# Kernel tuning notes

Measured on AMD Instinct MI355X. Metric: run time of the kernel, lower is better.

## Reference

```python
import jax, jax.numpy as jnp
import numpy as np
from jax import lax

L, B, N_IN, N_OUT, K = 1024, 16, 1024, 512, 5


def setup_inputs() -> dict:
    key = jax.random.key(0)
    k0, k1, k2, k3, k4 = jax.random.split(key, 5)
    val_range = (6.0 / (N_IN + N_OUT)) ** 0.5
    x = jax.random.normal(k0, (L, B, N_IN), dtype=jnp.float32)
    weight = jax.random.uniform(k1, (N_IN, N_OUT * K), dtype=jnp.float32,
                                minval=-val_range, maxval=val_range)
    bias = jax.random.normal(k2, (N_OUT * K,), dtype=jnp.float32) * 0.1
    bias_eps = jax.random.normal(k3, (N_OUT,), dtype=jnp.float32) * 0.1
    bias_final = jax.random.normal(k4, (N_OUT * 2,), dtype=jnp.float32) * 0.1
    return {"x": x, "weight": weight, "bias": bias,
            "bias_eps": bias_eps, "bias_final": bias_final}


def reference(x, weight, bias, bias_eps, bias_final):
    # x: [L, B, n_in]; unidirectional (bidir=1), real semiring, output gate, tanh
    length, batch, n_in = x.shape
    n_out = N_OUT
    u_ = (x.reshape(-1, n_in) @ weight).reshape(length, batch, n_out, K)
    b = bias.reshape(K, n_out)  # [5, n_out]: in1, in2, f1, f2, out
    forget_bias1, forget_bias2, output_bias = b[2], b[3], b[4]
    output = jax.nn.sigmoid(u_[..., 4] + output_bias)      # [L, B, n_out]
    forget1 = jax.nn.sigmoid(u_[..., 2] + forget_bias1)
    forget2 = jax.nn.sigmoid(u_[..., 3] + forget_bias2)
    u1, u2 = u_[..., 0], u_[..., 1]
    eps = jax.nn.sigmoid(bias_eps)                          # [n_out]

    def step(carry, inp):
        c1_prev, c2_prev = carry
        f1t, f2t, u1t, u2t = inp
        c1_t = c1_prev * f1t + u1t
        c2_t = c2_prev * f2t + (eps + c1_prev) * u2t
        return (c1_t, c2_t), (c1_t, c2_t)

    init = (jnp.zeros((batch, n_out), x.dtype), jnp.zeros((batch, n_out), x.dtype))
    (c1_final, c2_final), (c1s, c2s) = lax.scan(step, init, (forget1, forget2, u1, u2))

    rho = jax.nn.sigmoid(bias_final.reshape(n_out, 2)) * 2.0
    cs = c1s * rho[:, 0] + c2s * rho[:, 1]
    gcs = jnp.tanh(output * cs)                             # [L, B, n_out]
    return gcs, c1_final, c2_final
```

## Files before the change

kernel.cpp:

```cpp
#include <hip/hip_runtime.h>
#include <cstdint>

#define LSEQ 1024
#define BATCH 16
#define NIN 1024
#define NOUT 512
#define KGATE 5
#define NCOL (NOUT * KGATE)
#define MTOT (LSEQ * BATCH)
#define CHAINS (BATCH * NOUT)
#define OUT_GCS (LSEQ * BATCH * NOUT)
#define SEG 32
#define SLEN 32
#define PLANE ((size_t)MTOT * NOUT)
#define SMP ((size_t)SEG * CHAINS)

typedef _Float16 f16x8 __attribute__((ext_vector_type(8)));
typedef float f32x4 __attribute__((ext_vector_type(4)));

__device__ __forceinline__ void async16(const void* g, void* l) {
    __builtin_amdgcn_global_load_lds(
        (const __attribute__((address_space(1))) void*)(uintptr_t)g,
        (__attribute__((address_space(3))) void*)(uintptr_t)l,
        16, 0, 0);
}

__device__ __forceinline__ float fsigmoid(float x) {
    return 1.0f / (1.0f + __expf(-x));
}

__global__ void convert_x_k(const float* __restrict__ x, _Float16* __restrict__ xb, int n8) {
    int i = blockIdx.x * blockDim.x + threadIdx.x;
    if (i < n8) {
        float4 a = ((const float4*)x)[2 * i];
        float4 b = ((const float4*)x)[2 * i + 1];
        f16x8 h;
        h[0] = (_Float16)a.x; h[1] = (_Float16)a.y; h[2] = (_Float16)a.z; h[3] = (_Float16)a.w;
        h[4] = (_Float16)b.x; h[5] = (_Float16)b.y; h[6] = (_Float16)b.z; h[7] = (_Float16)b.w;
        ((f16x8*)xb)[i] = h;
    }
}

__global__ __launch_bounds__(256) void transpose_w_k(const float* __restrict__ w, _Float16* __restrict__ wT) {
    __shared__ float lds[32][33];
    int t = threadIdx.x;
    int col = t & 31;
    int rowg = t >> 5;
    int n0 = blockIdx.x * 32;
    int k0 = blockIdx.y * 32;
#pragma unroll
    for (int i = 0; i < 4; i++) {
        int r = rowg + i * 8;
        lds[r][col] = w[(size_t)(k0 + r) * NCOL + n0 + col];
    }
    __syncthreads();
#pragma unroll
    for (int i = 0; i < 4; i++) {
        int r = rowg + i * 8;
        int c = n0 + r;
        int row = (c % 5) * NOUT + (c / 5);
        wT[(size_t)row * NIN + k0 + col] = (_Float16)lds[col][r];
    }
}

__global__ __launch_bounds__(256, 2) void gemm_gates_k(const _Float16* __restrict__ A,
                                                       const _Float16* __restrict__ BT,
                                                       const float* __restrict__ bias,
                                                       _Float16* __restrict__ planes) {
    __shared__ _Float16 Al[256 * 64];
    __shared__ _Float16 Bl[128 * 64];
    int t = threadIdx.x;
    int w = t >> 6, lane = t & 63;
    int m0 = blockIdx.x * 256, n0 = blockIdx.y * 128;

    f32x4 acc[8][4] = {};

    const int q = lane >> 4, r16 = lane & 15;
    const int wm = (w >> 1) * 128, wn = (w & 1) * 64;

    for (int kk = 0; kk < NIN; kk += 64) {
#pragma unroll
        for (int cc = 0; cc < 8; cc++) {
            int c = t + cc * 256;
            int r = c >> 3, sg = c & 7;
            async16(A + (size_t)(m0 + r) * NIN + kk + sg * 8, (char*)Al + c * 16);
        }
#pragma unroll
        for (int cc = 0; cc < 4; cc++) {
            int c = t + cc * 256;
            int r = c >> 3, sg = c & 7;
            async16(BT + (size_t)(n0 + r) * NIN + kk + sg * 8, (char*)Bl + c * 16);
        }
        __syncthreads();

#pragma unroll
        for (int h = 0; h < 2; h++) {
            f16x8 af[8], bf[4];
#pragma unroll
            for (int i = 0; i < 8; i++)
                af[i] = *(const f16x8*)(Al + (wm + i * 16 + r16) * 64 + h * 32 + q * 8);
#pragma unroll
            for (int j = 0; j < 4; j++)
                bf[j] = *(const f16x8*)(Bl + (wn + j * 16 + r16) * 64 + h * 32 + q * 8);
#pragma unroll
            for (int i = 0; i < 8; i++)
#pragma unroll
                for (int j = 0; j < 4; j++)
                    acc[i][j] = __builtin_amdgcn_mfma_f32_16x16x32_f16(af[i], bf[j], acc[i][j], 0, 0, 0);
        }
        __syncthreads();
    }

    int g = n0 >> 9;
    int nb = n0 & (NOUT - 1);
    _Float16* plane = planes + (size_t)g * PLANE;
#pragma unroll
    for (int j = 0; j < 4; j++) {
        int coln = nb + wn + j * 16 + r16;
        float bv = bias[n0 + wn + j * 16 + r16];
#pragma unroll
        for (int i = 0; i < 8; i++) {
#pragma unroll
            for (int reg = 0; reg < 4; reg++) {
                int m = m0 + wm + i * 16 + q * 4 + reg;
                float v = acc[i][j][reg];
                if (g >= 2) v = fsigmoid(v + bv);
                plane[(size_t)m * NOUT + coln] = (_Float16)v;
            }
        }
    }
}

__global__ __launch_bounds__(256) void compose_k(const _Float16* __restrict__ planes,
                                                 const float* __restrict__ beps,
                                                 float* __restrict__ SM) {
    int u = blockIdx.x * 256 + threadIdx.x;
    int t = u & (CHAINS - 1);
    int s = u >> 13;
    int n = t & (NOUT - 1);
    float eps = fsigmoid(beps[n]);
    float a11 = 1.0f, a21 = 0.0f, a22 = 1.0f, b1 = 0.0f, b2 = 0.0f;
#pragma unroll 4
    for (int j = 0; j < SLEN; j++) {
        size_t e = (size_t)(s * SLEN + j) * CHAINS + t;
        float u1 = (float)planes[e];
        float u2 = (float)planes[PLANE + e];
        float f1 = (float)planes[2 * PLANE + e];
        float f2 = (float)planes[3 * PLANE + e];
        float na11 = f1 * a11;
        float na21 = fmaf(u2, a11, f2 * a21);
        float na22 = f2 * a22;
        float nb1  = fmaf(f1, b1, u1);
        float nb2  = fmaf(u2, b1, fmaf(f2, b2, eps * u2));
        a11 = na11; a21 = na21; a22 = na22; b1 = nb1; b2 = nb2;
    }
    size_t idx = (size_t)s * CHAINS + t;
    SM[idx] = a11;
    SM[SMP + idx] = a21;
    SM[2 * SMP + idx] = a22;
    SM[3 * SMP + idx] = b1;
    SM[4 * SMP + idx] = b2;
}

__global__ __launch_bounds__(256) void segscan_k(const float* __restrict__ SM,
                                                 float* __restrict__ segc,
                                                 float* __restrict__ out) {
    int t = blockIdx.x * 256 + threadIdx.x;
    float c1 = 0.0f, c2 = 0.0f;
#pragma unroll
    for (int s = 0; s < SEG; s++) {
        size_t idx = (size_t)s * CHAINS + t;
        segc[idx] = c1;
        segc[SMP + idx] = c2;
        float a11 = SM[idx];
        float a21 = SM[SMP + idx];
        float a22 = SM[2 * SMP + idx];
        float b1  = SM[3 * SMP + idx];
        float b2  = SM[4 * SMP + idx];
        float c1n = fmaf(a11, c1, b1);
        float c2n = fmaf(a21, c1, fmaf(a22, c2, b2));
        c1 = c1n; c2 = c2n;
    }
    out[OUT_GCS + t] = c1;
    out[OUT_GCS + CHAINS + t] = c2;
}

__global__ __launch_bounds__(256) void apply_k(const _Float16* __restrict__ planes,
                                               const float* __restrict__ segc,
                                               const float* __restrict__ beps,
                                               const float* __restrict__ bfin,
                                               float* __restrict__ out) {
    int u = blockIdx.x * 256 + threadIdx.x;
    int t = u & (CHAINS - 1);
    int s = u >> 13;
    int n = t & (NOUT - 1);
    float eps  = fsigmoid(beps[n]);
    float rho0 = 2.0f * fsigmoid(bfin[2 * n]);
    float rho1 = 2.0f * fsigmoid(bfin[2 * n + 1]);
    size_t idx = (size_t)s * CHAINS + t;
    float c1 = segc[idx];
    float c2 = segc[SMP + idx];
#pragma unroll 4
    for (int j = 0; j < SLEN; j++) {
        size_t e = (size_t)(s * SLEN + j) * CHAINS + t;
        float u1 = (float)planes[e];
        float u2 = (float)planes[PLANE + e];
        float f1 = (float)planes[2 * PLANE + e];
        float f2 = (float)planes[3 * PLANE + e];
        float o  = (float)planes[4 * PLANE + e];
        float c1p = c1;
        c1 = fmaf(c1p, f1, u1);
        c2 = fmaf(c2, f2, (eps + c1p) * u2);
        float cs = fmaf(c1, rho0, c2 * rho1);
        float y = o * cs;
        y = fminf(9.0f, fmaxf(-9.0f, y));
        float ex = __expf(2.0f * y);
        out[e] = (ex - 1.0f) / (ex + 1.0f);
    }
}

extern "C" void kernel_launch(void* const* d_in, const int* in_sizes, int n_in,
                              void* d_out, int out_size, void* d_ws, size_t ws_size,
                              hipStream_t stream) {
    const float* x    = (const float*)d_in[0];
    const float* wgt  = (const float*)d_in[1];
    const float* bias = (const float*)d_in[2];
    const float* beps = (const float*)d_in[3];
    const float* bfin = (const float*)d_in[4];
    float* out = (float*)d_out;

    char* p = (char*)d_ws;
    _Float16* wT     = (_Float16*)p; p += (size_t)NCOL * NIN * 2;
    _Float16* xb     = (_Float16*)p; p += (size_t)MTOT * NIN * 2;
    _Float16* planes = (_Float16*)p; p += 5 * PLANE * 2;
    float* SM        = (float*)p;    p += 5 * SMP * 4;
    float* segc      = (float*)p;    p += 2 * SMP * 4;

    transpose_w_k<<<dim3(NCOL / 32, NIN / 32), 256, 0, stream>>>(wgt, wT);

    int n8 = MTOT * NIN / 8;
    convert_x_k<<<dim3((n8 + 255) / 256), 256, 0, stream>>>(x, xb, n8);

    gemm_gates_k<<<dim3(MTOT / 256, NCOL / 128), 256, 0, stream>>>(xb, wT, bias, planes);

    compose_k<<<dim3(CHAINS * SEG / 256), 256, 0, stream>>>(planes, beps, SM);
    segscan_k<<<dim3(CHAINS / 256), 256, 0, stream>>>(SM, segc, out);
    apply_k<<<dim3(CHAINS * SEG / 256), 256, 0, stream>>>(planes, segc, beps, bfin, out);
}
```

Before: 285.8 us.

## Double-buffer swizzled GEMM tiles, vectorize epilogue, process two chains per thread in scans

```diff
diff --git a/kernel.cpp b/kernel.cpp
--- a/kernel.cpp
+++ b/kernel.cpp
@@ -15,7 +15,14 @@
 #define PLANE ((size_t)MTOT * NOUT)
 #define SMP ((size_t)SEG * CHAINS)
 
+#define BM 256
+#define BN 128
+#define BK 32
+#define NT (NIN / BK)
+
 typedef _Float16 f16x8 __attribute__((ext_vector_type(8)));
+typedef _Float16 f16x4 __attribute__((ext_vector_type(4)));
+typedef _Float16 f16x2 __attribute__((ext_vector_type(2)));
 typedef float f32x4 __attribute__((ext_vector_type(4)));
 
 __device__ __forceinline__ void async16(const void* g, void* l) {
@@ -63,70 +70,89 @@
     }
 }
 
-__global__ __launch_bounds__(256, 2) void gemm_gates_k(const _Float16* __restrict__ A,
+__global__ __launch_bounds__(256, 3) void gemm_gates_k(const _Float16* __restrict__ A,
                                                        const _Float16* __restrict__ BT,
                                                        const float* __restrict__ bias,
                                                        _Float16* __restrict__ planes) {
-    __shared__ _Float16 Al[256 * 64];
-    __shared__ _Float16 Bl[128 * 64];
-    int t = threadIdx.x;
-    int w = t >> 6, lane = t & 63;
-    int m0 = blockIdx.x * 256, n0 = blockIdx.y * 128;
-
-    f32x4 acc[8][4] = {};
-
+    __shared__ _Float16 lds[24576];
+    const int t = threadIdx.x;
+    const int w = t >> 6, lane = t & 63;
     const int q = lane >> 4, r16 = lane & 15;
     const int wm = (w >> 1) * 128, wn = (w & 1) * 64;
-
-    for (int kk = 0; kk < NIN; kk += 64) {
-#pragma unroll
-        for (int cc = 0; cc < 8; cc++) {
-            int c = t + cc * 256;
-            int r = c >> 3, sg = c & 7;
-            async16(A + (size_t)(m0 + r) * NIN + kk + sg * 8, (char*)Al + c * 16);
-        }
-#pragma unroll
-        for (int cc = 0; cc < 4; cc++) {
-            int c = t + cc * 256;
-            int r = c >> 3, sg = c & 7;
-            async16(BT + (size_t)(n0 + r) * NIN + kk + sg * 8, (char*)Bl + c * 16);
-        }
+    const int m0 = blockIdx.x * BM, n0 = blockIdx.y * BN;
+
+    const int swz = (q ^ ((r16 >> 1) & 3)) << 4;
+    const int aBase = (wm + r16) * 64 + swz;
+    const int bBase = 32768 + (wn + r16) * 64 + swz;
+
+    const int rS = t >> 2;
+    const int skS = (t & 3) ^ ((rS >> 1) & 3);
+    const _Float16* aS = A + (size_t)(m0 + rS) * NIN + skS * 8;
+    const _Float16* bS = BT + (size_t)(n0 + rS) * NIN + skS * 8;
+    char* const ldsb = (char*)lds;
+    const int aDst = t * 16;
+    const int bDst = 32768 + t * 16;
+
+    auto stage = [&](int tile, int nxt) {
+        const _Float16* ap = aS + (size_t)tile * BK;
+        const _Float16* bp = bS + (size_t)tile * BK;
+#pragma unroll
+        for (int L = 0; L < 4; L++)
+            async16(ap + (size_t)L * 64 * NIN, ldsb + nxt * 16384 + aDst + L * 4096);
+#pragma unroll
+        for (int L = 0; L < 2; L++)
+            async16(bp + (size_t)L * 64 * NIN, ldsb + nxt * 8192 + bDst + L * 4096);
+    };
+
+    f32x4 acc[8][4] = {};
+
+    stage(0, 0);
+    __syncthreads();
+
+#pragma unroll 2
+    for (int tt = 0; tt < NT; tt++) {
+        const int cur = tt & 1;
+        if (tt + 1 < NT) stage(tt + 1, cur ^ 1);
+
+        f16x8 af[8], bf[4];
+        const char* ab = ldsb + cur * 16384 + aBase;
+        const char* bb = ldsb + cur * 8192 + bBase;
+#pragma unroll
+        for (int i = 0; i < 8; i++) af[i] = *(const f16x8*)(ab + i * 1024);
+#pragma unroll
+        for (int j = 0; j < 4; j++) bf[j] = *(const f16x8*)(bb + j * 1024);
+
+        __builtin_amdgcn_s_setprio(1);
+#pragma unroll
+        for (int i = 0; i < 8; i++)
+#pragma unroll
+            for (int j = 0; j < 4; j++)
+                acc[i][j] = __builtin_amdgcn_mfma_f32_16x16x32_f16(bf[j], af[i], acc[i][j], 0, 0, 0);
+        __builtin_amdgcn_s_setprio(0);
+
         __syncthreads();
-
-#pragma unroll
-        for (int h = 0; h < 2; h++) {
-            f16x8 af[8], bf[4];
-#pragma unroll
-            for (int i = 0; i < 8; i++)
-                af[i] = *(const f16x8*)(Al + (wm + i * 16 + r16) * 64 + h * 32 + q * 8);
-#pragma unroll
-            for (int j = 0; j < 4; j++)
-                bf[j] = *(const f16x8*)(Bl + (wn + j * 16 + r16) * 64 + h * 32 + q * 8);
-#pragma unroll
-            for (int i = 0; i < 8; i++)
-#pragma unroll
-                for (int j = 0; j < 4; j++)
-                    acc[i][j] = __builtin_amdgcn_mfma_f32_16x16x32_f16(af[i], bf[j], acc[i][j], 0, 0, 0);
-        }
-        __syncthreads();
-    }
-
-    int g = n0 >> 9;
-    int nb = n0 & (NOUT - 1);
+    }
+
+    const int g = n0 >> 9;
+    const int nb = n0 & (NOUT - 1);
     _Float16* plane = planes + (size_t)g * PLANE;
 #pragma unroll
-    for (int j = 0; j < 4; j++) {
-        int coln = nb + wn + j * 16 + r16;
-        float bv = bias[n0 + wn + j * 16 + r16];
-#pragma unroll
-        for (int i = 0; i < 8; i++) {
+    for (int i = 0; i < 8; i++) {
+        int m = m0 + wm + i * 16 + r16;
+        _Float16* prow = plane + (size_t)m * NOUT + nb;
+#pragma unroll
+        for (int j = 0; j < 4; j++) {
+            int nn = wn + j * 16 + q * 4;
+            float4 bv = *(const float4*)(bias + n0 + nn);
+            f16x4 hv;
 #pragma unroll
             for (int reg = 0; reg < 4; reg++) {
-                int m = m0 + wm + i * 16 + q * 4 + reg;
                 float v = acc[i][j][reg];
-                if (g >= 2) v = fsigmoid(v + bv);
-                plane[(size_t)m * NOUT + coln] = (_Float16)v;
+                float b = (reg == 0) ? bv.x : (reg == 1) ? bv.y : (reg == 2) ? bv.z : bv.w;
+                if (g >= 2) v = fsigmoid(v + b);
+                hv[reg] = (_Float16)v;
             }
+            *(f16x4*)(prow + nn) = hv;
         }
     }
 }
@@ -135,31 +161,42 @@
                                                  const float* __restrict__ beps,
                                                  float* __restrict__ SM) {
     int u = blockIdx.x * 256 + threadIdx.x;
-    int t = u & (CHAINS - 1);
-    int s = u >> 13;
-    int n = t & (NOUT - 1);
-    float eps = fsigmoid(beps[n]);
-    float a11 = 1.0f, a21 = 0.0f, a22 = 1.0f, b1 = 0.0f, b2 = 0.0f;
+    int t2 = u & (CHAINS / 2 - 1);
+    int s = u >> 12;
+    int tch = t2 << 1;
+    int n = tch & (NOUT - 1);
+    float eps[2] = { fsigmoid(beps[n]), fsigmoid(beps[n + 1]) };
+    float a11[2] = {1.0f, 1.0f}, a21[2] = {}, a22[2] = {1.0f, 1.0f}, b1[2] = {}, b2[2] = {};
+    const f16x2* p2 = (const f16x2*)planes;
+    const size_t P2E = PLANE >> 1;
+    const size_t estep = CHAINS >> 1;
+    size_t e = ((size_t)(s * SLEN) * CHAINS + tch) >> 1;
+    f16x2 u1n = p2[e], u2n = p2[P2E + e], f1n = p2[2 * P2E + e], f2n = p2[3 * P2E + e];
 #pragma unroll 4
     for (int j = 0; j < SLEN; j++) {
-        size_t e = (size_t)(s * SLEN + j) * CHAINS + t;
-        float u1 = (float)planes[e];
-        float u2 = (float)planes[PLANE + e];
-        float f1 = (float)planes[2 * PLANE + e];
-        float f2 = (float)planes[3 * PLANE + e];
-        float na11 = f1 * a11;
-        float na21 = fmaf(u2, a11, f2 * a21);
-        float na22 = f2 * a22;
-        float nb1  = fmaf(f1, b1, u1);
-        float nb2  = fmaf(u2, b1, fmaf(f2, b2, eps * u2));
-        a11 = na11; a21 = na21; a22 = na22; b1 = nb1; b2 = nb2;
-    }
-    size_t idx = (size_t)s * CHAINS + t;
-    SM[idx] = a11;
-    SM[SMP + idx] = a21;
-    SM[2 * SMP + idx] = a22;
-    SM[3 * SMP + idx] = b1;
-    SM[4 * SMP + idx] = b2;
+        f16x2 u1c = u1n, u2c = u2n, f1c = f1n, f2c = f2n;
+        if (j + 1 < SLEN) {
+            e += estep;
+            u1n = p2[e]; u2n = p2[P2E + e]; f1n = p2[2 * P2E + e]; f2n = p2[3 * P2E + e];
+        }
+#pragma unroll
+        for (int c = 0; c < 2; c++) {
+            float u1 = (float)u1c[c], u2 = (float)u2c[c];
+            float f1 = (float)f1c[c], f2 = (float)f2c[c];
+            float na11 = f1 * a11[c];
+            float na21 = fmaf(u2, a11[c], f2 * a21[c]);
+            float na22 = f2 * a22[c];
+            float nb1  = fmaf(f1, b1[c], u1);
+            float nb2  = fmaf(u2, b1[c], fmaf(f2, b2[c], eps[c] * u2));
+            a11[c] = na11; a21[c] = na21; a22[c] = na22; b1[c] = nb1; b2[c] = nb2;
+        }
+    }
+    size_t idx = (size_t)s * CHAINS + tch;
+    *(float2*)(SM + idx)           = make_float2(a11[0], a11[1]);
+    *(float2*)(SM + SMP + idx)     = make_float2(a21[0], a21[1]);
+    *(float2*)(SM + 2 * SMP + idx) = make_float2(a22[0], a22[1]);
+    *(float2*)(SM + 3 * SMP + idx) = make_float2(b1[0], b1[1]);
+    *(float2*)(SM + 4 * SMP + idx) = make_float2(b2[0], b2[1]);
 }
 
 __global__ __launch_bounds__(256) void segscan_k(const float* __restrict__ SM,
@@ -167,16 +204,19 @@
                                                  float* __restrict__ out) {
     int t = blockIdx.x * 256 + threadIdx.x;
     float c1 = 0.0f, c2 = 0.0f;
+    float a11n = SM[t], a21n = SM[SMP + t], a22n = SM[2 * SMP + t];
+    float b1n = SM[3 * SMP + t], b2n = SM[4 * SMP + t];
 #pragma unroll
     for (int s = 0; s < SEG; s++) {
+        float a11 = a11n, a21 = a21n, a22 = a22n, b1 = b1n, b2 = b2n;
+        if (s + 1 < SEG) {
+            size_t nx = (size_t)(s + 1) * CHAINS + t;
+            a11n = SM[nx]; a21n = SM[SMP + nx]; a22n = SM[2 * SMP + nx];
+            b1n = SM[3 * SMP + nx]; b2n = SM[4 * SMP + nx];
+        }
         size_t idx = (size_t)s * CHAINS + t;
         segc[idx] = c1;
         segc[SMP + idx] = c2;
-        float a11 = SM[idx];
-        float a21 = SM[SMP + idx];
-        float a22 = SM[2 * SMP + idx];
-        float b1  = SM[3 * SMP + idx];
-        float b2  = SM[4 * SMP + idx];
         float c1n = fmaf(a11, c1, b1);
         float c2n = fmaf(a21, c1, fmaf(a22, c2, b2));
         c1 = c1n; c2 = c2n;
@@ -191,31 +231,53 @@
                                                const float* __restrict__ bfin,
                                                float* __restrict__ out) {
     int u = blockIdx.x * 256 + threadIdx.x;
-    int t = u & (CHAINS - 1);
-    int s = u >> 13;
-    int n = t & (NOUT - 1);
-    float eps  = fsigmoid(beps[n]);
-    float rho0 = 2.0f * fsigmoid(bfin[2 * n]);
-    float rho1 = 2.0f * fsigmoid(bfin[2 * n + 1]);
-    size_t idx = (size_t)s * CHAINS + t;
-    float c1 = segc[idx];
-    float c2 = segc[SMP + idx];
+    int t2 = u & (CHAINS / 2 - 1);
+    int s = u >> 12;
+    int tch = t2 << 1;
+    int n = tch & (NOUT - 1);
+    float eps[2], rho0[2], rho1[2], c1[2], c2[2];
+#pragma unroll
+    for (int c = 0; c < 2; c++) {
+        eps[c]  = fsigmoid(beps[n + c]);
+        rho0[c] = 2.0f * fsigmoid(bfin[2 * (n + c)]);
+        rho1[c] = 2.0f * fsigmoid(bfin[2 * (n + c) + 1]);
+    }
+    size_t idx = (size_t)s * CHAINS + tch;
+    float2 c1v = *(const float2*)(segc + idx);
+    float2 c2v = *(const float2*)(segc + SMP + idx);
+    c1[0] = c1v.x; c1[1] = c1v.y; c2[0] = c2v.x; c2[1] = c2v.y;
+    const f16x2* p2 = (const f16x2*)planes;
+    const size_t P2E = PLANE >> 1;
+    const size_t estep = CHAINS >> 1;
+    size_t e2 = ((size_t)(s * SLEN) * CHAINS + tch) >> 1;
+    size_t eo = (size_t)(s * SLEN) * CHAINS + tch;
+    f16x2 u1n = p2[e2], u2n = p2[P2E + e2], f1n = p2[2 * P2E + e2],
+          f2n = p2[3 * P2E + e2], on = p2[4 * P2E + e2];
 #pragma unroll 4
     for (int j = 0; j < SLEN; j++) {
-        size_t e = (size_t)(s * SLEN + j) * CHAINS + t;
-        float u1 = (float)planes[e];
-        float u2 = (float)planes[PLANE + e];
-        float f1 = (float)planes[2 * PLANE + e];
-        float f2 = (float)planes[3 * PLANE + e];
-        float o  = (float)planes[4 * PLANE + e];
-        float c1p = c1;
-        c1 = fmaf(c1p, f1, u1);
-        c2 = fmaf(c2, f2, (eps + c1p) * u2);
-        float cs = fmaf(c1, rho0, c2 * rho1);
-        float y = o * cs;
-        y = fminf(9.0f, fmaxf(-9.0f, y));
-        float ex = __expf(2.0f * y);
-        out[e] = (ex - 1.0f) / (ex + 1.0f);
+        f16x2 u1c = u1n, u2c = u2n, f1c = f1n, f2c = f2n, oc = on;
+        if (j + 1 < SLEN) {
+            e2 += estep;
+            u1n = p2[e2]; u2n = p2[P2E + e2]; f1n = p2[2 * P2E + e2];
+            f2n = p2[3 * P2E + e2]; on = p2[4 * P2E + e2];
+        }
+        float yr[2];
+#pragma unroll
+        for (int c = 0; c < 2; c++) {
+            float u1 = (float)u1c[c], u2 = (float)u2c[c];
+            float f1 = (float)f1c[c], f2 = (float)f2c[c];
+            float o  = (float)oc[c];
+            float c1p = c1[c];
+            c1[c] = fmaf(c1p, f1, u1);
+            c2[c] = fmaf(c2[c], f2, (eps[c] + c1p) * u2);
+            float cs = fmaf(c1[c], rho0[c], c2[c] * rho1[c]);
+            float y = o * cs;
+            y = fminf(9.0f, fmaxf(-9.0f, y));
+            float ex = __expf(2.0f * y);
+            yr[c] = (ex - 1.0f) / (ex + 1.0f);
+        }
+        *(float2*)(out + eo) = make_float2(yr[0], yr[1]);
+        eo += CHAINS;
     }
 }
 
@@ -241,9 +303,9 @@
     int n8 = MTOT * NIN / 8;
     convert_x_k<<<dim3((n8 + 255) / 256), 256, 0, stream>>>(x, xb, n8);
 
-    gemm_gates_k<<<dim3(MTOT / 256, NCOL / 128), 256, 0, stream>>>(xb, wT, bias, planes);
-
-    compose_k<<<dim3(CHAINS * SEG / 256), 256, 0, stream>>>(planes, beps, SM);
+    gemm_gates_k<<<dim3(MTOT / BM, NCOL / BN), 256, 0, stream>>>(xb, wT, bias, planes);
+
+    compose_k<<<dim3(SEG * CHAINS / 2 / 256), 256, 0, stream>>>(planes, beps, SM);
     segscan_k<<<dim3(CHAINS / 256), 256, 0, stream>>>(SM, segc, out);
-    apply_k<<<dim3(CHAINS * SEG / 256), 256, 0, stream>>>(planes, segc, beps, bfin, out);
-}
+    apply_k<<<dim3(SEG * CHAINS / 2 / 256), 256, 0, stream>>>(planes, segc, beps, bfin, out);
+}
```

Measured after the change: 414.6 us. 1.45x slower.
